# Performance work log

Measured on AMD Instinct MI355X. Metric: run time of the kernel, lower is better.

Reference implementation:

```python
import jax, jax.numpy as jnp
import numpy as np

N, M_DIM, CTRL = 16384, 512, 1024
EPS = 1e-16

def setup_inputs() -> dict:
    key = jax.random.key(0)
    k1, k2, k3, k4, k5 = jax.random.split(key, 5)
    embeddings = jax.random.normal(k1, (1, CTRL), dtype=jnp.float32)
    w_prev = jax.random.uniform(k2, (1, N), dtype=jnp.float32)
    w_prev = w_prev / jnp.sum(w_prev, axis=1, keepdims=True)  # valid soft address
    memory = jax.random.normal(k3, (N, M_DIM), dtype=jnp.float32) * 0.05
    out_f = 3 * M_DIM + 6  # write_lengths = [M,1,1,3,1,M,M]
    W = jax.random.normal(k4, (out_f, CTRL), dtype=jnp.float32) * (1.0 / np.sqrt(CTRL))
    b = jax.random.normal(k5, (out_f,), dtype=jnp.float32) * 0.01
    return {"embeddings": embeddings, "w_prev": w_prev, "memory": memory, "W": W, "b": b}

def reference(embeddings, w_prev, memory, W, b):
    Md = memory.shape[1]
    o = (embeddings @ W.T + b).reshape(1, -1)  # [1, 3M+6]
    # column split per write_lengths [M,1,1,3,1,M,M]
    k = o[:, :Md]
    beta = jax.nn.softplus(o[:, Md:Md + 1])
    g = jax.nn.sigmoid(o[:, Md + 1:Md + 2])
    s = jax.nn.softmax(o[:, Md + 2:Md + 5], axis=1)       # 3 circular shifts
    gamma = 1.0 + jax.nn.softplus(o[:, Md + 5:Md + 6])
    e = o[:, Md + 6:2 * Md + 6]                            # erase vector [1,M]
    a = o[:, 2 * Md + 6:]                                  # add vector   [1,M]
    # content addressing: cosine similarity of k against each memory row
    mem_norm = jnp.linalg.norm(memory, axis=1)             # [N]
    k_norm = jnp.linalg.norm(k, axis=1)                    # [1]
    sim = (k @ memory.T) / (k_norm[:, None] * mem_norm[None, :] + EPS)  # [1,N]
    wc = jax.nn.softmax(beta * sim, axis=1)
    # interpolation with previous weights
    wg = g * wc + (1.0 - g) * w_prev
    # circular convolution with 3-tap shift kernel (shifts -1,0,+1)
    ws = (s[:, 0:1] * jnp.roll(wg, 1, axis=1)
          + s[:, 1:2] * wg
          + s[:, 2:3] * jnp.roll(wg, -1, axis=1))
    # sharpening
    wp = jnp.power(ws + EPS, gamma)
    w = wp / jnp.sum(wp, axis=1, keepdims=True)            # [1,N]
    # erase/add outer-product memory write
    erase = w.T @ e                                        # [N,M]
    add = w.T @ a                                          # [N,M]
    new_memory = memory * (1.0 - erase) + add
    return w, new_memory
```

## Files before the change

kernel.cpp:

```cpp
#include <hip/hip_runtime.h>
#include <math.h>

#define N 16384
#define MD 512
#define CTRLDIM 1024
#define OUTF 1542


__device__ __forceinline__ float softplus_f(float x) {
    return (x > 20.f) ? x : log1pf(expf(x));
}

__device__ __forceinline__ float wave_bfly_sum(float v) {
    #pragma unroll
    for (int off = 1; off < 64; off <<= 1) v += __shfl_xor(v, off, 64);
    return v;
}

__global__ void k_proj(const float* __restrict__ emb, const float* __restrict__ W,
                       const float* __restrict__ b, float* __restrict__ O,
                       float* __restrict__ E, float* __restrict__ A) {
    int row = blockIdx.x;
    int t = threadIdx.x;
    const float4* w4 = (const float4*)(W + (size_t)row * CTRLDIM);
    const float4* e4 = (const float4*)emb;
    float4 wv = w4[t];
    float4 ev = e4[t];
    float p = wv.x * ev.x + wv.y * ev.y + wv.z * ev.z + wv.w * ev.w;
    p = wave_bfly_sum(p);
    __shared__ float s[4];
    int lane = t & 63, wid = t >> 6;
    if (lane == 0) s[wid] = p;
    __syncthreads();
    if (t == 0) {
        float val = s[0] + s[1] + s[2] + s[3] + b[row];
        O[row] = val;
        if (row >= MD + 6 && row < 2 * MD + 6)      E[row - (MD + 6)] = val;
        else if (row >= 2 * MD + 6)                 A[row - (2 * MD + 6)] = val;
    }
}

__global__ void __launch_bounds__(256) k_sim(const float* __restrict__ mem,
                                             const float* __restrict__ O,
                                             float* __restrict__ EZ,
                                             float* __restrict__ PART1) {
    int t = threadIdx.x, lane = t & 63, wid = t >> 6;
    const float4* k4 = (const float4*)O;
    float4 k0 = k4[lane], k1 = k4[lane + 64];
    float ksq = k0.x * k0.x + k0.y * k0.y + k0.z * k0.z + k0.w * k0.w
              + k1.x * k1.x + k1.y * k1.y + k1.z * k1.z + k1.w * k1.w;
    ksq = wave_bfly_sum(ksq);
    float knorm = sqrtf(ksq);
    float beta = softplus_f(O[MD]);
    int row0 = (blockIdx.x * 4 + wid) * 8;
    float4 m0[8], m1[8];
    #pragma unroll
    for (int r = 0; r < 8; r++) {
        const float4* m4 = (const float4*)(mem + (size_t)(row0 + r) * MD);
        m0[r] = m4[lane];
        m1[r] = m4[lane + 64];
    }
    float wsum = 0.f;
    #pragma unroll
    for (int r = 0; r < 8; r++) {
        float dot = m0[r].x * k0.x + m0[r].y * k0.y + m0[r].z * k0.z + m0[r].w * k0.w
                  + m1[r].x * k1.x + m1[r].y * k1.y + m1[r].z * k1.z + m1[r].w * k1.w;
        float nsq = m0[r].x * m0[r].x + m0[r].y * m0[r].y + m0[r].z * m0[r].z + m0[r].w * m0[r].w
                  + m1[r].x * m1[r].x + m1[r].y * m1[r].y + m1[r].z * m1[r].z + m1[r].w * m1[r].w;
        dot = wave_bfly_sum(dot);
        nsq = wave_bfly_sum(nsq);
        float z = beta * dot / (knorm * sqrtf(nsq) + 1e-16f);
        float ez = expf(z - beta);
        if (lane == r) EZ[row0 + r] = ez;
        wsum += ez;
    }
    __shared__ float sblk[4];
    if (lane == 0) sblk[wid] = wsum;
    __syncthreads();
    if (t == 0) PART1[blockIdx.x] = sblk[0] + sblk[1] + sblk[2] + sblk[3];
}

__global__ void __launch_bounds__(256) k_shift(const float* __restrict__ EZ,
                                               const float* __restrict__ wprev,
                                               const float* __restrict__ O,
                                               const float* __restrict__ PART1,
                                               float* __restrict__ WP,
                                               float* __restrict__ PART2) {
    int t = threadIdx.x, lane = t & 63, wid = t >> 6;
    float v = 0.f;
    #pragma unroll
    for (int j = 0; j < 8; j++) v += PART1[lane + j * 64];
    float inv1 = 1.f / wave_bfly_sum(v);
    float g = 1.f / (1.f + expf(-O[MD + 1]));
    float s0r = O[MD + 2], s1r = O[MD + 3], s2r = O[MD + 4];
    float m = fmaxf(s0r, fmaxf(s1r, s2r));
    float e0 = expf(s0r - m), e1 = expf(s1r - m), e2 = expf(s2r - m);
    float inv_se = 1.f / (e0 + e1 + e2);
    float s0 = e0 * inv_se, s1 = e1 * inv_se, s2 = e2 * inv_se;
    float gamma = 1.f + softplus_f(O[MD + 5]);
    float gm1 = 1.f - g;
    int i = blockIdx.x * 256 + t;
    int im = (i == 0) ? (N - 1) : (i - 1);
    int ip = (i == N - 1) ? 0 : (i + 1);
    float wgm = g * EZ[im] * inv1 + gm1 * wprev[im];
    float wgc = g * EZ[i]  * inv1 + gm1 * wprev[i];
    float wgp = g * EZ[ip] * inv1 + gm1 * wprev[ip];
    float wsv = s0 * wgm + s1 * wgc + s2 * wgp;
    float wp = exp2f(gamma * log2f(wsv + 1e-16f));
    WP[i] = wp;
    float bs = wave_bfly_sum(wp);
    __shared__ float sblk[4];
    if (lane == 0) sblk[wid] = bs;
    __syncthreads();
    if (t == 0) PART2[blockIdx.x] = sblk[0] + sblk[1] + sblk[2] + sblk[3];
}

__global__ void __launch_bounds__(256) k_upd(const float* __restrict__ mem,
                                             const float* __restrict__ WP,
                                             const float* __restrict__ PART2,
                                             const float* __restrict__ E,
                                             const float* __restrict__ A,
                                             float* __restrict__ wout,
                                             float* __restrict__ outMem) {
    int t = threadIdx.x, lane = t & 63;
    float inv2 = 1.f / wave_bfly_sum(PART2[lane]);
    const float4* m4 = (const float4*)mem;
    const float4* e4 = (const float4*)E;
    const float4* a4 = (const float4*)A;
    float4* o4 = (float4*)outMem;
    #pragma unroll
    for (int it = 0; it < 2; it++) {
        int idx = (blockIdx.x * 2 + it) * 256 + t;
        int i = idx >> 7;
        int c = idx & 127;
        float wi = WP[i] * inv2;
        if (c == 0) wout[i] = wi;
        float4 mv = m4[idx];
        float4 e = e4[c];
        float4 a = a4[c];
        float4 o;
        o.x = mv.x * (1.f - wi * e.x) + wi * a.x;
        o.y = mv.y * (1.f - wi * e.y) + wi * a.y;
        o.z = mv.z * (1.f - wi * e.z) + wi * a.z;
        o.w = mv.w * (1.f - wi * e.w) + wi * a.w;
        o4[idx] = o;
    }
}

extern "C" void kernel_launch(void* const* d_in, const int* in_sizes, int n_in,
                              void* d_out, int out_size, void* d_ws, size_t ws_size,
                              hipStream_t stream) {
    const float* emb   = (const float*)d_in[0];
    const float* wprev = (const float*)d_in[1];
    const float* mem   = (const float*)d_in[2];
    const float* W     = (const float*)d_in[3];
    const float* b     = (const float*)d_in[4];
    float* out = (float*)d_out;
    float* wsf = (float*)d_ws;
    float* O     = wsf;
    float* E     = wsf + 1552;
    float* A     = wsf + 2064;
    float* PART1 = wsf + 2576;
    float* PART2 = wsf + 3600;
    float* EZ    = wsf + 3664;
    float* WP    = wsf + 20048;

    k_proj<<<OUTF, 256, 0, stream>>>(emb, W, b, O, E, A);
    k_sim<<<N / 32, 256, 0, stream>>>(mem, O, EZ, PART1);
    k_shift<<<N / 256, 256, 0, stream>>>(EZ, wprev, O, PART1, WP, PART2);
    k_upd<<<(N * (MD / 4)) / 512, 256, 0, stream>>>(mem, WP, PART2, E, A, out, out + N);
}
```

Before: 111.2 us.

## Fuse shift/sharpen and memory update into one kernel with redundant normalization

Merges the shift/sharpen kernel and the erase/add update kernel into a single 256-block, 512-thread kernel. Every block recomputes all N sharpened weights to get the global normalizer, so no separate launch or grid-wide reduction is needed, and it keeps only its own 64 weights in LDS for the 64 memory rows it updates. This removes one launch and the WP/PART2 round trips through global memory. In exchange every block reads all of EZ and wprev and does N log/exp evaluations, which adds redundant work before the bandwidth-bound update starts.

```diff
diff --git a/kernel.cpp b/kernel.cpp
--- a/kernel.cpp
+++ b/kernel.cpp
@@ -80,17 +80,24 @@
     if (t == 0) PART1[blockIdx.x] = sblk[0] + sblk[1] + sblk[2] + sblk[3];
 }
 
-__global__ void __launch_bounds__(256) k_shift(const float* __restrict__ EZ,
-                                               const float* __restrict__ wprev,
-                                               const float* __restrict__ O,
-                                               const float* __restrict__ PART1,
-                                               float* __restrict__ WP,
-                                               float* __restrict__ PART2) {
+__global__ void __launch_bounds__(512) k_supd(const float* __restrict__ mem,
+                                              const float* __restrict__ EZ,
+                                              const float* __restrict__ wprev,
+                                              const float* __restrict__ O,
+                                              const float* __restrict__ PART1,
+                                              const float* __restrict__ E,
+                                              const float* __restrict__ A,
+                                              float* __restrict__ wout,
+                                              float* __restrict__ outMem) {
     int t = threadIdx.x, lane = t & 63, wid = t >> 6;
-    float v = 0.f;
-    #pragma unroll
-    for (int j = 0; j < 8; j++) v += PART1[lane + j * 64];
+    int b = blockIdx.x;
+    __shared__ float lds_wp[64];
+    __shared__ float sblk[8];
+
+    float v = PART1[lane] + PART1[lane + 64] + PART1[lane + 128] + PART1[lane + 192]
+            + PART1[lane + 256] + PART1[lane + 320] + PART1[lane + 384] + PART1[lane + 448];
     float inv1 = 1.f / wave_bfly_sum(v);
+
     float g = 1.f / (1.f + expf(-O[MD + 1]));
     float s0r = O[MD + 2], s1r = O[MD + 3], s2r = O[MD + 4];
     float m = fmaxf(s0r, fmaxf(s1r, s2r));
@@ -99,42 +106,41 @@
     float s0 = e0 * inv_se, s1 = e1 * inv_se, s2 = e2 * inv_se;
     float gamma = 1.f + softplus_f(O[MD + 5]);
     float gm1 = 1.f - g;
-    int i = blockIdx.x * 256 + t;
-    int im = (i == 0) ? (N - 1) : (i - 1);
-    int ip = (i == N - 1) ? 0 : (i + 1);
-    float wgm = g * EZ[im] * inv1 + gm1 * wprev[im];
-    float wgc = g * EZ[i]  * inv1 + gm1 * wprev[i];
-    float wgp = g * EZ[ip] * inv1 + gm1 * wprev[ip];
-    float wsv = s0 * wgm + s1 * wgc + s2 * wgp;
-    float wp = exp2f(gamma * log2f(wsv + 1e-16f));
-    WP[i] = wp;
-    float bs = wave_bfly_sum(wp);
-    __shared__ float sblk[4];
+
+    int jmine = b >> 3;
+    int tlo = (b & 7) * 64;
+    float sum2 = 0.f;
+    #pragma unroll 4
+    for (int j = 0; j < N / 512; j++) {
+        int i = j * 512 + t;
+        int im = (i == 0) ? (N - 1) : (i - 1);
+        int ip = (i == N - 1) ? 0 : (i + 1);
+        float wgm = g * EZ[im] * inv1 + gm1 * wprev[im];
+        float wgc = g * EZ[i]  * inv1 + gm1 * wprev[i];
+        float wgp = g * EZ[ip] * inv1 + gm1 * wprev[ip];
+        float wsv = s0 * wgm + s1 * wgc + s2 * wgp;
+        float wp = exp2f(gamma * log2f(wsv + 1e-16f));
+        sum2 += wp;
+        if (j == jmine && t >= tlo && t < tlo + 64) lds_wp[t - tlo] = wp;
+    }
+    float bs = wave_bfly_sum(sum2);
     if (lane == 0) sblk[wid] = bs;
     __syncthreads();
-    if (t == 0) PART2[blockIdx.x] = sblk[0] + sblk[1] + sblk[2] + sblk[3];
-}
+    float inv2 = 1.f / (sblk[0] + sblk[1] + sblk[2] + sblk[3]
+                      + sblk[4] + sblk[5] + sblk[6] + sblk[7]);
 
-__global__ void __launch_bounds__(256) k_upd(const float* __restrict__ mem,
-                                             const float* __restrict__ WP,
-                                             const float* __restrict__ PART2,
-                                             const float* __restrict__ E,
-                                             const float* __restrict__ A,
-                                             float* __restrict__ wout,
-                                             float* __restrict__ outMem) {
-    int t = threadIdx.x, lane = t & 63;
-    float inv2 = 1.f / wave_bfly_sum(PART2[lane]);
+    if (t < 64) wout[b * 64 + t] = lds_wp[t] * inv2;
+
     const float4* m4 = (const float4*)mem;
     const float4* e4 = (const float4*)E;
     const float4* a4 = (const float4*)A;
     float4* o4 = (float4*)outMem;
-    #pragma unroll
-    for (int it = 0; it < 2; it++) {
-        int idx = (blockIdx.x * 2 + it) * 256 + t;
-        int i = idx >> 7;
-        int c = idx & 127;
-        float wi = WP[i] * inv2;
-        if (c == 0) wout[i] = wi;
+    #pragma unroll 4
+    for (int it = 0; it < 16; it++) {
+        int local = it * 512 + t;
+        int idx = b * 8192 + local;
+        float wi = lds_wp[local >> 7] * inv2;
+        int c = local & 127;
         float4 mv = m4[idx];
         float4 e = e4[c];
         float4 a = a4[c];
@@ -161,12 +167,9 @@
     float* E     = wsf + 1552;
     float* A     = wsf + 2064;
     float* PART1 = wsf + 2576;
-    float* PART2 = wsf + 3600;
     float* EZ    = wsf + 3664;
-    float* WP    = wsf + 20048;
 
     k_proj<<<OUTF, 256, 0, stream>>>(emb, W, b, O, E, A);
     k_sim<<<N / 32, 256, 0, stream>>>(mem, O, EZ, PART1);
-    k_shift<<<N / 256, 256, 0, stream>>>(EZ, wprev, O, PART1, WP, PART2);
-    k_upd<<<(N * (MD / 4)) / 512, 256, 0, stream>>>(mem, WP, PART2, E, A, out, out + N);
+    k_supd<<<256, 512, 0, stream>>>(mem, EZ, wprev, O, PART1, E, A, out, out + N);
 }
```

Result: slower. 119.9 us (+7.9%).
